# Kernel tuning notes

Measured on AMD Instinct MI355X. Metric: run time of the kernel, lower is better.

The kernel has to match this reference:

```python
import jax, jax.numpy as jnp
import numpy as np

NUM_USER = 100000
K = 32
DIM = 64

def setup_inputs() -> dict:
    key = jax.random.key(0)
    k1, k2, k3 = jax.random.split(key, 3)
    features = jax.random.normal(k1, (NUM_USER, DIM), dtype=jnp.float32)
    user_graph = jax.random.randint(k2, (NUM_USER, K), 0, NUM_USER, dtype=jnp.int64)
    user_matrix = jax.random.uniform(k3, (NUM_USER, K), dtype=jnp.float32)
    return {"features": features, "user_graph": user_graph, "user_matrix": user_matrix}

def reference(features, user_graph, user_matrix):
    # u_features: [num_user, k, dim] gather of neighbor features
    u_features = features[user_graph]
    # weighted sum over k neighbors: [num_user, k] x [num_user, k, dim] -> [num_user, dim]
    u_pre = jnp.einsum('nk,nkd->nd', user_matrix, u_features)
    return u_pre
```

## Files before the change

kernel.cpp:

```cpp
#include <hip/hip_runtime.h>
#include <hip/hip_bf16.h>

#define NUM_USER 100000
#define K_NEIGH 32
#define DIM 64

typedef float floatx2 __attribute__((ext_vector_type(2)));

__global__ __launch_bounds__(256) void convert_bf16_kernel(
    const floatx2* __restrict__ feat2,
    unsigned int*  __restrict__ table) {
  int i = blockIdx.x * blockDim.x + threadIdx.x;
  if (i >= NUM_USER * DIM / 2) return;
  floatx2 f = feat2[i];
  unsigned int ux = __float_as_uint(f.x);
  unsigned int uy = __float_as_uint(f.y);
  unsigned int bx = (ux + 0x7fffu + ((ux >> 16) & 1u)) >> 16;
  unsigned int by = (uy + 0x7fffu + ((uy >> 16) & 1u)) >> 16;
  table[i] = bx | (by << 16);
}

__global__ __launch_bounds__(256) void user_graph_gather_bf16_kernel(
    const unsigned int* __restrict__ table,
    const int*          __restrict__ graph,
    const float*        __restrict__ matrix,
    floatx2*            __restrict__ out2) {
  int t  = blockIdx.x * blockDim.x + threadIdx.x;
  int u  = t >> 5;
  int d2 = t & 31;
  if (u >= NUM_USER) return;

  const int*   g = graph  + u * K_NEIGH;
  const float* w = matrix + u * K_NEIGH;

  float acc0 = 0.f, acc1 = 0.f;
#pragma unroll
  for (int k = 0; k < K_NEIGH; ++k) {
    int   idx = g[k];
    float wk  = w[k];
    unsigned int p = table[idx * 32 + d2];
    float flo = __uint_as_float(p << 16);
    float fhi = __uint_as_float(p & 0xffff0000u);
    acc0 += wk * flo;
    acc1 += wk * fhi;
  }
  floatx2 r; r.x = acc0; r.y = acc1;
  out2[u * 32 + d2] = r;
}

__global__ __launch_bounds__(256) void user_graph_gather_f32_kernel(
    const float* __restrict__ features,
    const int*   __restrict__ graph,
    const float* __restrict__ matrix,
    float*       __restrict__ out) {
  int t = blockIdx.x * blockDim.x + threadIdx.x;
  int u = t >> 6;
  int d = t & 63;
  if (u >= NUM_USER) return;
  const int*   g = graph  + (size_t)u * K_NEIGH;
  const float* w = matrix + (size_t)u * K_NEIGH;
  float acc = 0.f;
#pragma unroll
  for (int k = 0; k < K_NEIGH; ++k)
    acc += w[k] * features[(size_t)g[k] * DIM + d];
  out[(size_t)u * DIM + d] = acc;
}

extern "C" void kernel_launch(void* const* d_in, const int* in_sizes, int n_in,
                              void* d_out, int out_size, void* d_ws, size_t ws_size,
                              hipStream_t stream) {
  const float* features = (const float*)d_in[0];
  const int*   graph    = (const int*)d_in[1];
  const float* matrix   = (const float*)d_in[2];

  const size_t table_bytes = (size_t)NUM_USER * DIM * 2;
  if (ws_size >= table_bytes) {
    unsigned int* table = (unsigned int*)d_ws;
    const int n_pack = NUM_USER * DIM / 2;
    convert_bf16_kernel<<<(n_pack + 255) / 256, 256, 0, stream>>>(
        (const floatx2*)features, table);
    const int total = NUM_USER * 32;
    user_graph_gather_bf16_kernel<<<(total + 255) / 256, 256, 0, stream>>>(
        table, graph, matrix, (floatx2*)d_out);
  } else {
    const int total = NUM_USER * DIM;
    user_graph_gather_f32_kernel<<<(total + 255) / 256, 256, 0, stream>>>(
        features, graph, matrix, (float*)d_out);
  }
}
```

Measured before the change: 138.6 us.

## Fuse bf16 conversion and gather into one cooperative persistent kernel

Merges the bf16 table conversion and the neighbor gather into a single cooperative kernel with a grid-wide sync, using a grid-stride persistent loop. Each lane loads one graph index and one weight, and the values are broadcast with wavefront shuffles instead of every lane reading all 32. Nontemporal loads and stores are used for streaming data. This is meant to remove a kernel launch and the redundant index and weight loads, at the cost of a grid sync and a hardcoded 256-CU grid size. If the cooperative launch fails it falls back to the two-kernel path.

```diff
diff --git a/kernel.cpp b/kernel.cpp
--- a/kernel.cpp
+++ b/kernel.cpp
@@ -1,11 +1,64 @@
 #include <hip/hip_runtime.h>
-#include <hip/hip_bf16.h>
+#include <hip/hip_cooperative_groups.h>
 
 #define NUM_USER 100000
 #define K_NEIGH 32
 #define DIM 64
 
+namespace cg = cooperative_groups;
+
 typedef float floatx2 __attribute__((ext_vector_type(2)));
+typedef float floatx4 __attribute__((ext_vector_type(4)));
+typedef unsigned int uintx2 __attribute__((ext_vector_type(2)));
+
+__device__ __forceinline__ unsigned int pack_bf16(float a, float b) {
+  unsigned int ua = __float_as_uint(a), ub = __float_as_uint(b);
+  unsigned int ra = (ua + 0x7fffu + ((ua >> 16) & 1u)) >> 16;
+  unsigned int rb = (ub + 0x7fffu + ((ub >> 16) & 1u)) >> 16;
+  return ra | (rb << 16);
+}
+
+__global__ __launch_bounds__(256, 8) void fused_convert_gather_kernel(
+    const floatx4* __restrict__ feat4,
+    unsigned int*  __restrict__ table,
+    const int*     __restrict__ graph,
+    const float*   __restrict__ matrix,
+    floatx2*       __restrict__ out2) {
+  const int tid    = blockIdx.x * blockDim.x + threadIdx.x;
+  const int stride = gridDim.x * blockDim.x;
+
+  uintx2* table2 = (uintx2*)table;
+  for (int i = tid; i < NUM_USER * DIM / 4; i += stride) {
+    floatx4 f = __builtin_nontemporal_load(feat4 + i);
+    uintx2 r;
+    r.x = pack_bf16(f.x, f.y);
+    r.y = pack_bf16(f.z, f.w);
+    table2[i] = r;
+  }
+
+  cg::this_grid().sync();
+
+  const int total = NUM_USER * 32;
+  for (int t = tid; t < total; t += stride) {
+    const int u  = t >> 5;
+    const int d2 = t & 31;
+
+    int   myg = __builtin_nontemporal_load(graph  + u * K_NEIGH + d2);
+    float myw = __builtin_nontemporal_load(matrix + u * K_NEIGH + d2);
+
+    float acc0 = 0.f, acc1 = 0.f;
+#pragma unroll
+    for (int k = 0; k < K_NEIGH; ++k) {
+      int   idx = __shfl(myg, k, 32);
+      float wk  = __shfl(myw, k, 32);
+      unsigned int p = table[idx * 32 + d2];
+      acc0 += wk * __uint_as_float(p << 16);
+      acc1 += wk * __uint_as_float(p & 0xffff0000u);
+    }
+    floatx2 r; r.x = acc0; r.y = acc1;
+    __builtin_nontemporal_store(r, out2 + t);
+  }
+}
 
 __global__ __launch_bounds__(256) void convert_bf16_kernel(
     const floatx2* __restrict__ feat2,
@@ -13,11 +66,7 @@
   int i = blockIdx.x * blockDim.x + threadIdx.x;
   if (i >= NUM_USER * DIM / 2) return;
   floatx2 f = feat2[i];
-  unsigned int ux = __float_as_uint(f.x);
-  unsigned int uy = __float_as_uint(f.y);
-  unsigned int bx = (ux + 0x7fffu + ((ux >> 16) & 1u)) >> 16;
-  unsigned int by = (uy + 0x7fffu + ((uy >> 16) & 1u)) >> 16;
-  table[i] = bx | (by << 16);
+  table[i] = pack_bf16(f.x, f.y);
 }
 
 __global__ __launch_bounds__(256) void user_graph_gather_bf16_kernel(
@@ -29,20 +78,16 @@
   int u  = t >> 5;
   int d2 = t & 31;
   if (u >= NUM_USER) return;
-
   const int*   g = graph  + u * K_NEIGH;
   const float* w = matrix + u * K_NEIGH;
-
   float acc0 = 0.f, acc1 = 0.f;
 #pragma unroll
   for (int k = 0; k < K_NEIGH; ++k) {
     int   idx = g[k];
     float wk  = w[k];
     unsigned int p = table[idx * 32 + d2];
-    float flo = __uint_as_float(p << 16);
-    float fhi = __uint_as_float(p & 0xffff0000u);
-    acc0 += wk * flo;
-    acc1 += wk * fhi;
+    acc0 += wk * __uint_as_float(p << 16);
+    acc1 += wk * __uint_as_float(p & 0xffff0000u);
   }
   floatx2 r; r.x = acc0; r.y = acc1;
   out2[u * 32 + d2] = r;
@@ -76,6 +121,26 @@
   const size_t table_bytes = (size_t)NUM_USER * DIM * 2;
   if (ws_size >= table_bytes) {
     unsigned int* table = (unsigned int*)d_ws;
+
+    static int bpc = 0;
+    if (bpc == 0) {
+      int q = 0;
+      hipError_t e = hipOccupancyMaxActiveBlocksPerMultiprocessor(
+          &q, fused_convert_gather_kernel, 256, 0);
+      bpc = (e == hipSuccess && q > 0) ? q : 4;
+      if (bpc > 8) bpc = 8;
+    }
+    int nblk = bpc * 256;
+
+    const floatx4* feat4 = (const floatx4*)features;
+    floatx2*       o2    = (floatx2*)d_out;
+    void* args[] = {(void*)&feat4, (void*)&table, (void*)&graph,
+                    (void*)&matrix, (void*)&o2};
+    hipError_t e = hipLaunchCooperativeKernel(
+        fused_convert_gather_kernel, dim3(nblk), dim3(256), args, 0, stream);
+    if (e == hipSuccess) return;
+
+    (void)hipGetLastError();
     const int n_pack = NUM_USER * DIM / 2;
     convert_bf16_kernel<<<(n_pack + 255) / 256, 256, 0, stream>>>(
         (const floatx2*)features, table);
```

New measurement: 221.5 us. 59.8% more time.

## Drop bf16 table pre-pass; gather fp32 directly with LDS-staged neighbor indices

Applied to the files above, without the earlier changes.

Removes the separate fp32-to-bf16 conversion kernel and the reduced-precision gather, and gathers fp32 features directly as float2 per thread. Each block stages its 8 users' neighbor indices and weights into shared memory with one coalesced nontemporal load per thread, replacing the per-thread broadcast global loads. The output is written with nontemporal stores. This saves a full pass over the feature table and restores exact fp32 accuracy, but doubles the bytes per random gather compared with the bf16 table.

```diff
diff --git a/kernel.cpp b/kernel.cpp
--- a/kernel.cpp
+++ b/kernel.cpp
@@ -1,69 +1,45 @@
 #include <hip/hip_runtime.h>
-#include <hip/hip_bf16.h>
 
 #define NUM_USER 100000
 #define K_NEIGH 32
 #define DIM 64
+#define USERS_PER_BLOCK 8
 
 typedef float floatx2 __attribute__((ext_vector_type(2)));
 
-__global__ __launch_bounds__(256) void convert_bf16_kernel(
+__global__ __launch_bounds__(256) void gather_f32_lds_kernel(
     const floatx2* __restrict__ feat2,
-    unsigned int*  __restrict__ table) {
-  int i = blockIdx.x * blockDim.x + threadIdx.x;
-  if (i >= NUM_USER * DIM / 2) return;
-  floatx2 f = feat2[i];
-  unsigned int ux = __float_as_uint(f.x);
-  unsigned int uy = __float_as_uint(f.y);
-  unsigned int bx = (ux + 0x7fffu + ((ux >> 16) & 1u)) >> 16;
-  unsigned int by = (uy + 0x7fffu + ((uy >> 16) & 1u)) >> 16;
-  table[i] = bx | (by << 16);
-}
+    const int*     __restrict__ graph,
+    const float*   __restrict__ matrix,
+    floatx2*       __restrict__ out2) {
+  __shared__ int2 pairs[USERS_PER_BLOCK * K_NEIGH];
 
-__global__ __launch_bounds__(256) void user_graph_gather_bf16_kernel(
-    const unsigned int* __restrict__ table,
-    const int*          __restrict__ graph,
-    const float*        __restrict__ matrix,
-    floatx2*            __restrict__ out2) {
-  int t  = blockIdx.x * blockDim.x + threadIdx.x;
-  int u  = t >> 5;
-  int d2 = t & 31;
-  if (u >= NUM_USER) return;
+  const int e    = threadIdx.x;
+  const int base = blockIdx.x * (USERS_PER_BLOCK * K_NEIGH);
 
-  const int*   g = graph  + u * K_NEIGH;
-  const float* w = matrix + u * K_NEIGH;
+  int   gv = __builtin_nontemporal_load(graph  + base + e);
+  float wv = __builtin_nontemporal_load(matrix + base + e);
+  pairs[e] = make_int2(gv, __float_as_int(wv));
+  __syncthreads();
+
+  const int u_local = e >> 5;
+  const int d2      = e & 31;
+  const int u       = blockIdx.x * USERS_PER_BLOCK + u_local;
+
+  const int2* prow = pairs + u_local * K_NEIGH;
 
   float acc0 = 0.f, acc1 = 0.f;
 #pragma unroll
   for (int k = 0; k < K_NEIGH; ++k) {
-    int   idx = g[k];
-    float wk  = w[k];
-    unsigned int p = table[idx * 32 + d2];
-    float flo = __uint_as_float(p << 16);
-    float fhi = __uint_as_float(p & 0xffff0000u);
-    acc0 += wk * flo;
-    acc1 += wk * fhi;
+    int2  pr = prow[k];
+    float wk = __int_as_float(pr.y);
+    floatx2 p = feat2[pr.x * 32 + d2];
+    acc0 += wk * p.x;
+    acc1 += wk * p.y;
   }
+
   floatx2 r; r.x = acc0; r.y = acc1;
-  out2[u * 32 + d2] = r;
-}
-
-__global__ __launch_bounds__(256) void user_graph_gather_f32_kernel(
-    const float* __restrict__ features,
-    const int*   __restrict__ graph,
-    const float* __restrict__ matrix,
-    float*       __restrict__ out) {
-  int t = blockIdx.x * blockDim.x + threadIdx.x;
-  int u = t >> 6;
-  int d = t & 63;
-  if (u >= NUM_USER) return;
-  const int*   g = graph  + (size_t)u * K_NEIGH;
-  const float* w = matrix + (size_t)u * K_NEIGH;
-  float acc = 0.f;
-#pragma unroll
-  for (int k = 0; k < K_NEIGH; ++k)
-    acc += w[k] * features[(size_t)g[k] * DIM + d];
-  out[(size_t)u * DIM + d] = acc;
+  __builtin_nontemporal_store(r, out2 + u * 32 + d2);
 }
 
 extern "C" void kernel_launch(void* const* d_in, const int* in_sizes, int n_in,
@@ -73,18 +49,6 @@
   const int*   graph    = (const int*)d_in[1];
   const float* matrix   = (const float*)d_in[2];
 
-  const size_t table_bytes = (size_t)NUM_USER * DIM * 2;
-  if (ws_size >= table_bytes) {
-    unsigned int* table = (unsigned int*)d_ws;
-    const int n_pack = NUM_USER * DIM / 2;
-    convert_bf16_kernel<<<(n_pack + 255) / 256, 256, 0, stream>>>(
-        (const floatx2*)features, table);
-    const int total = NUM_USER * 32;
-    user_graph_gather_bf16_kernel<<<(total + 255) / 256, 256, 0, stream>>>(
-        table, graph, matrix, (floatx2*)d_out);
-  } else {
-    const int total = NUM_USER * DIM;
-    user_graph_gather_f32_kernel<<<(total + 255) / 256, 256, 0, stream>>>(
-        features, graph, matrix, (float*)d_out);
-  }
+  gather_f32_lds_kernel<<<NUM_USER / USERS_PER_BLOCK, 256, 0, stream>>>(
+      (const floatx2*)features, graph, matrix, (floatx2*)d_out);
 }
```

New measurement: 178.8 us. +29.0%, slower.
